# Kernel tuning notes

Measured on AMD Instinct MI355X. Metric: run time of the kernel, lower is better.

The kernel has to match this reference:

```python
import jax, jax.numpy as jnp
import numpy as np

BOUNDS = (0, 256, 384, 448, 512)  # rot_idx, trans_idx, angle_idx, embedding_dim
SCALES = [1, 2, 4, 8, 16, 32, 64]  # 2**i for i in range(scales+1), scales=6


def _pairwise_dist(q, e):
    # q: [M, C] queries, e: [K, C] codebook; per-segment squared dist / seg_dim, summed
    d = jnp.zeros((q.shape[0], e.shape[0]), dtype=q.dtype)
    for s, t in zip(BOUNDS[:-1], BOUNDS[1:]):
        qs, es = q[:, s:t], e[:, s:t]
        d = d + (jnp.sum(qs * qs, axis=1, keepdims=True)
                 + jnp.sum(es * es, axis=1)
                 - 2.0 * qs @ es.T) / (t - s)
    return d


def _elem_dist(q, k):
    # q, k: [B, C, N]; elementwise per-segment squared distance / seg_dim -> [B, N]
    d = 0.0
    for s, t in zip(BOUNDS[:-1], BOUNDS[1:]):
        diff = q[:, s:t] - k[:, s:t]
        d = d + jnp.sum(diff * diff, axis=1) / (t - s)
    return d


def _downsample_area(f, pn):
    # f: [B, C, N], pn divides N -> block-mean pooling (torch 'area')
    B, C, N = f.shape
    return f.reshape(B, C, pn, N // pn).mean(axis=-1)


def _upsample_linear(h, N):
    # h: [B, C, pn] -> [B, C, N], torch mode='linear', align_corners=False
    pn = h.shape[-1]
    src = (jnp.arange(N, dtype=jnp.float32) + 0.5) * (pn / N) - 0.5
    src = jnp.clip(src, 0.0, pn - 1)
    i0 = jnp.floor(src).astype(jnp.int32)
    i1 = jnp.minimum(i0 + 1, pn - 1)
    w = (src - i0).astype(h.dtype)
    return h[..., i0] * (1.0 - w) + h[..., i1] * w


def setup_inputs() -> dict:
    key = jax.random.key(0)
    k1, k2, k3 = jax.random.split(key, 3)
    C = 512
    f_BNC = jax.random.normal(k1, (1024, 64, C), dtype=jnp.float32)
    base = jax.random.normal(k2, (2048, C), dtype=jnp.float32)
    proj_W = jax.random.normal(k3, (C, C), dtype=jnp.float32) / np.sqrt(C)
    return {"f_BNC": f_BNC, "base": base, "proj_W": proj_W}


def reference(f_BNC, base, proj_W):
    embedding = base @ proj_W.T              # update_embedding(): proj(base)
    emb_ng = jax.lax.stop_gradient(embedding)
    f_BCN = jnp.transpose(f_BNC, (0, 2, 1))  # [B, C, N]
    B, C, N = f_BCN.shape
    f_no_grad = jax.lax.stop_gradient(f_BCN)
    f_rest = f_no_grad
    f_hat = jnp.zeros_like(f_rest)
    commit = jnp.zeros((B, N), dtype=f_BCN.dtype)
    qlat = jnp.zeros((B, N), dtype=f_BCN.dtype)
    for pn in SCALES:
        rest_NC = jnp.transpose(_downsample_area(f_rest, pn), (0, 2, 1)).reshape(-1, C)
        d = _pairwise_dist(jax.lax.stop_gradient(rest_NC), emb_ng)  # [B*pn, K]
        idx = jnp.argmin(d, axis=1)
        h_NC = embedding[idx]                                        # gather (grad -> codebook)
        h_BCn = jnp.transpose(h_NC.reshape(B, pn, C), (0, 2, 1))
        h_BCN = _upsample_linear(h_BCn, N)
        f_hat = f_hat + h_BCN
        f_rest = f_rest - h_BCN
        commit = commit + 0.25 * _elem_dist(jax.lax.stop_gradient(f_hat), f_BCN)
        qlat = qlat + _elem_dist(f_hat, f_no_grad)
    SN = float(len(SCALES))
    commit = commit / SN
    qlat = qlat / SN
    f_hat_st = jax.lax.stop_gradient(f_hat) - f_no_grad + f_BCN  # straight-through
    return (jnp.transpose(f_hat_st, (0, 2, 1)), commit, qlat)
```

## Files before the change

### kernel.cpp

```cpp
#include <hip/hip_runtime.h>

typedef __attribute__((ext_vector_type(8))) _Float16 f16x8;
typedef __attribute__((ext_vector_type(4))) float f32x4;

#define B_    1024
#define C_    512
#define NCODE 2048
#define NTOT  (B_ * 64 * C_)
#define BN_   (B_ * 64)
#define DELTA 3e-3f

__device__ __forceinline__ float wseg(int k) {
    return k < 256 ? (1.0f / 256.0f) : (k < 384 ? (1.0f / 128.0f) : (1.0f / 64.0f));
}

__global__ __launch_bounds__(256) void k_gemm_e(const float* __restrict__ A,
                                                const float* __restrict__ Bm,
                                                float* __restrict__ E) {
    __shared__ float As[16][68];
    __shared__ float Bs[16][68];
    int tid = threadIdx.x;
    int m0 = blockIdx.x * 64, n0 = blockIdx.y * 64;
    float acc[4][4] = {};
    int tx = tid & 15, ty = tid >> 4;
    int kk = tid & 15, rr = tid >> 4;
    for (int k0 = 0; k0 < 512; k0 += 16) {
        #pragma unroll
        for (int i = 0; i < 4; ++i) {
            As[kk][rr + i * 16] = A[(m0 + rr + i * 16) * 512 + k0 + kk];
            Bs[kk][rr + i * 16] = Bm[(n0 + rr + i * 16) * 512 + k0 + kk];
        }
        __syncthreads();
        #pragma unroll
        for (int k = 0; k < 16; ++k) {
            float4 a = *(const float4*)&As[k][ty * 4];
            float4 b = *(const float4*)&Bs[k][tx * 4];
            #pragma unroll
            for (int i = 0; i < 4; ++i) {
                float av = ((const float*)&a)[i];
                acc[i][0] = fmaf(av, b.x, acc[i][0]);
                acc[i][1] = fmaf(av, b.y, acc[i][1]);
                acc[i][2] = fmaf(av, b.z, acc[i][2]);
                acc[i][3] = fmaf(av, b.w, acc[i][3]);
            }
        }
        __syncthreads();
    }
    #pragma unroll
    for (int i = 0; i < 4; ++i)
        #pragma unroll
        for (int j = 0; j < 4; ++j)
            E[(m0 + ty * 4 + i) * 512 + n0 + tx * 4 + j] = acc[i][j];
}

__global__ void k_wek16(const float* __restrict__ E, _Float16* __restrict__ wk) {
    int tid = blockIdx.x * 256 + threadIdx.x;
    int k = tid & 511;
    wk[tid] = (_Float16)(E[tid] * wseg(k));
}

__global__ void k_enorm(const float* __restrict__ E, float* __restrict__ enorm) {
    int c = blockIdx.x * 256 + threadIdx.x;
    float s = 0.0f;
    for (int k = 0; k < 512; ++k) {
        float v = E[c * 512 + k];
        s = fmaf(wseg(k) * v, v, s);
    }
    enorm[c] = s;
}

__global__ __launch_bounds__(256) void k_down0(const float* __restrict__ f,
                                               _Float16* __restrict__ q16,
                                               float* __restrict__ qf) {
    int b = blockIdx.x, t = threadIdx.x;
    const float* src = f + (size_t)b * 64 * 512;
    float s0 = 0.f, s1 = 0.f;
    for (int n = 0; n < 64; ++n) {
        s0 += src[n * 512 + t];
        s1 += src[n * 512 + t + 256];
    }
    s0 *= (1.0f / 64.0f); s1 *= (1.0f / 64.0f);
    q16[(size_t)b * 512 + t] = (_Float16)s0;
    q16[(size_t)b * 512 + t + 256] = (_Float16)s1;
    qf[(size_t)b * 512 + t] = s0;
    qf[(size_t)b * 512 + t + 256] = s1;
}

__global__ __launch_bounds__(256, 4) void k_score_f16(
        const _Float16* __restrict__ q16, const _Float16* __restrict__ wek,
        const float* __restrict__ enorm, float4* __restrict__ partial) {
    __shared__ __align__(16) char smem[37376];
    float*  ensh = (float*)(smem + 32768);
    float4* bb   = (float4*)(smem + 33280);

    int tid = threadIdx.x;
    int bx = blockIdx.x;
    int m0 = blockIdx.y * 128, n0 = bx * 128;
    if (tid < 128) ensh[tid] = enorm[n0 + tid];

    int lane = tid & 63, wave = tid >> 6;
    int wrow = (wave & 1) * 64, wcol = (wave >> 1) * 64;
    int lx = lane & 15, cg = lane >> 4;

    int r0 = tid >> 2, c0 = tid & 3;
    int cs0 = (c0 ^ (r0 & 3)) * 8;
    const _Float16* gqa0 = q16 + (size_t)(m0 + r0) * 512 + cs0;
    const _Float16* gqa1 = q16 + (size_t)(m0 + 64 + r0) * 512 + cs0;
    const _Float16* gwb0 = wek + (size_t)(n0 + r0) * 512 + cs0;
    const _Float16* gwb1 = wek + (size_t)(n0 + 64 + r0) * 512 + cs0;

    #define GLL(gp, loff) __builtin_amdgcn_global_load_lds( \
        (const __attribute__((address_space(1))) unsigned int*)(gp), \
        (__attribute__((address_space(3))) unsigned int*)(smem + (loff)), 16, 0, 0)

    auto stage = [&](int p, int k0) {
        GLL(gqa0 + k0, p * 8192 + tid * 16);
        GLL(gqa1 + k0, p * 8192 + 4096 + tid * 16);
        GLL(gwb0 + k0, 16384 + p * 8192 + tid * 16);
        GLL(gwb1 + k0, 16384 + p * 8192 + 4096 + tid * 16);
    };

    f32x4 acc[4][4];
    #pragma unroll
    for (int i = 0; i < 4; ++i)
        #pragma unroll
        for (int j = 0; j < 4; ++j)
            acc[i][j] = (f32x4){0.f, 0.f, 0.f, 0.f};

    int abase = (wrow + lx) * 64 + ((cg ^ (lx & 3)) * 16);
    int bbase = (wcol + lx) * 64 + ((cg ^ (lx & 3)) * 16);

    stage(0, 0);
    __syncthreads();

    #pragma unroll
    for (int ks = 0; ks < 16; ++ks) {
        int p = ks & 1;
        if (ks < 15) stage(p ^ 1, (ks + 1) * 32);
        f16x8 af[4], bf[4];
        #pragma unroll
        for (int i = 0; i < 4; ++i) {
            af[i] = *(const f16x8*)(smem + p * 8192 + abase + i * 1024);
            bf[i] = *(const f16x8*)(smem + 16384 + p * 8192 + bbase + i * 1024);
        }
        #pragma unroll
        for (int i = 0; i < 4; ++i)
            #pragma unroll
            for (int j = 0; j < 4; ++j)
                acc[i][j] = __builtin_amdgcn_mfma_f32_16x16x32_f16(af[i], bf[j], acc[i][j], 0, 0, 0);
        __syncthreads();
    }

    #pragma unroll
    for (int fi = 0; fi < 4; ++fi) {
        #pragma unroll
        for (int r = 0; r < 4; ++r) {
            float v1 = INFINITY, v2 = INFINITY; int i1 = NCODE, i2 = NCODE;
            #pragma unroll
            for (int fj = 0; fj < 4; ++fj) {
                int nl = wcol + fj * 16 + lx;
                float s = ensh[nl] - 2.0f * acc[fi][fj][r];
                int code = n0 + nl;
                if (s < v1) { v2 = v1; i2 = i1; v1 = s; i1 = code; }
                else if (s < v2) { v2 = s; i2 = code; }
            }
            #pragma unroll
            for (int d = 1; d < 16; d <<= 1) {
                float ov1 = __shfl_xor(v1, d), ov2 = __shfl_xor(v2, d);
                int oi1 = __shfl_xor(i1, d), oi2 = __shfl_xor(i2, d);
                if (ov1 < v1) {
                    if (v1 < ov2) { v2 = v1; i2 = i1; } else { v2 = ov2; i2 = oi2; }
                    v1 = ov1; i1 = oi1;
                } else if (ov1 < v2) { v2 = ov1; i2 = oi1; }
            }
            if (lx == 0) {
                int row = wrow + fi * 16 + cg * 4 + r;
                bb[row * 2 + (wave >> 1)] = make_float4(v1, __int_as_float(i1),
                                                        v2, __int_as_float(i2));
            }
        }
    }
    __syncthreads();
    if (tid < 128) {
        float4 A4 = bb[tid * 2], C4 = bb[tid * 2 + 1];
        float v1, v2; int i1, i2;
        if (A4.x <= C4.x) {
            v1 = A4.x; i1 = __float_as_int(A4.y);
            if (A4.z <= C4.x) { v2 = A4.z; i2 = __float_as_int(A4.w); }
            else { v2 = C4.x; i2 = __float_as_int(C4.y); }
        } else {
            v1 = C4.x; i1 = __float_as_int(C4.y);
            if (C4.z <= A4.x) { v2 = C4.z; i2 = __float_as_int(C4.w); }
            else { v2 = A4.x; i2 = __float_as_int(A4.y); }
        }
        partial[(size_t)(m0 + tid) * 16 + bx] =
            make_float4(v1, __int_as_float(i1), v2, __int_as_float(i2));
    }
}

__global__ __launch_bounds__(256) void k_rescue(
        const float4* __restrict__ partial, const float* __restrict__ qf,
        const float* __restrict__ E, const float* __restrict__ enorm,
        int* __restrict__ idxb) {
    int wid = (blockIdx.x * 256 + threadIdx.x) >> 6;
    int lane = threadIdx.x & 63;
    float4 p;
    if (lane < 16) p = partial[(size_t)wid * 16 + lane];
    else p = make_float4(INFINITY, __int_as_float(NCODE), INFINITY, __int_as_float(NCODE));
    float bv = p.x;
    #pragma unroll
    for (int d = 1; d < 64; d <<= 1) bv = fminf(bv, __shfl_xor(bv, d));
    float thresh = bv + DELTA;
    unsigned long long m1 = __ballot(lane < 16 && p.x <= thresh);
    unsigned long long m2 = __ballot(lane < 16 && p.z <= thresh);
    const float* q = qf + (size_t)wid * 512 + lane * 8;
    float4 q0 = *(const float4*)q;
    float4 q1 = *(const float4*)(q + 4);
    float w = wseg(lane * 8);
    float qw0 = q0.x * w, qw1 = q0.y * w, qw2 = q0.z * w, qw3 = q0.w * w;
    float qw4 = q1.x * w, qw5 = q1.y * w, qw6 = q1.z * w, qw7 = q1.w * w;
    float bs = INFINITY; int bi = NCODE;
    while (m1 | m2) {
        int ci;
        if (m1) {
            int src = __ffsll((long long)m1) - 1; m1 &= m1 - 1;
            ci = __shfl(__float_as_int(p.y), src);
        } else {
            int src = __ffsll((long long)m2) - 1; m2 &= m2 - 1;
            ci = __shfl(__float_as_int(p.w), src);
        }
        const float* e = E + (size_t)ci * 512 + lane * 8;
        float4 e0 = *(const float4*)e;
        float4 e1 = *(const float4*)(e + 4);
        float a = 0.f;
        a = fmaf(qw0, e0.x, a); a = fmaf(qw1, e0.y, a);
        a = fmaf(qw2, e0.z, a); a = fmaf(qw3, e0.w, a);
        a = fmaf(qw4, e1.x, a); a = fmaf(qw5, e1.y, a);
        a = fmaf(qw6, e1.z, a); a = fmaf(qw7, e1.w, a);
        #pragma unroll
        for (int d = 1; d < 64; d <<= 1) a += __shfl_xor(a, d);
        float s = enorm[ci] - 2.0f * a;
        if (s < bs || (s == bs && ci < bi)) { bs = s; bi = ci; }
    }
    if (lane == 0) idxb[wid] = bi;
}

__global__ __launch_bounds__(256) void k_update(
        const float* __restrict__ E, const int* __restrict__ idx,
        const float* __restrict__ f, float* __restrict__ rest,
        float* __restrict__ dacc, _Float16* __restrict__ q16n,
        float* __restrict__ qf32n, int pn, int sn, int mode) {
    int t = threadIdx.x;
    int pn_next = 1 << sn;
    int r = 64 >> sn;
    int b = blockIdx.x >> sn;
    int chunk = blockIdx.x & (pn_next - 1);
    float w0 = wseg(t), w1 = wseg(t + 256);
    float macc0 = 0.f, macc1 = 0.f;
    float pscale = (float)pn * (1.0f / 64.0f);
    __shared__ float redw[4];
    for (int ri = 0; ri < r; ++ri) {
        int n = chunk * r + ri;
        int row = (b << 6) + n;
        float srcp = fminf(fmaxf((n + 0.5f) * pscale - 0.5f, 0.0f), (float)(pn - 1));
        int i0 = (int)floorf(srcp);
        int i1 = min(i0 + 1, pn - 1);
        float wl = srcp - (float)i0;
        int cc0 = idx[b * pn + i0];
        int cc1 = idx[b * pn + i1];
        const float* e0 = E + (size_t)cc0 * 512;
        const float* e1 = E + (size_t)cc1 * 512;
        const float* rs = (mode & 1) ? f + (size_t)row * 512 : rest + (size_t)row * 512;
        float s = 0.f;
        {
            float h = (1.0f - wl) * e0[t] + wl * e1[t];
            float v = rs[t] - h;
            rest[(size_t)row * 512 + t] = (mode & 2) ? (f[(size_t)row * 512 + t] - v) : v;
            s = fmaf(w0 * v, v, s);
            macc0 += v;
        }
        {
            int c = t + 256;
            float h = (1.0f - wl) * e0[c] + wl * e1[c];
            float v = rs[c] - h;
            rest[(size_t)row * 512 + c] = (mode & 2) ? (f[(size_t)row * 512 + c] - v) : v;
            s = fmaf(w1 * v, v, s);
            macc1 += v;
        }
        #pragma unroll
        for (int d = 1; d < 64; d <<= 1) s += __shfl_xor(s, d);
        if ((t & 63) == 0) redw[t >> 6] = s;
        __syncthreads();
        if (t == 0) {
            float tot = redw[0] + redw[1] + redw[2] + redw[3];
            dacc[row] = (mode & 1) ? tot : dacc[row] + tot;
        }
        __syncthreads();
    }
    if (!(mode & 2)) {
        float inv = 1.0f / (float)r;
        size_t qrow = ((size_t)b << sn) + chunk;
        float m0v = macc0 * inv, m1v = macc1 * inv;
        q16n[qrow * 512 + t] = (_Float16)m0v;
        q16n[qrow * 512 + t + 256] = (_Float16)m1v;
        if (mode & 4) {
            qf32n[qrow * 512 + t] = m0v;
            qf32n[qrow * 512 + t + 256] = m1v;
        }
    }
}

__global__ void k_out12(const float* __restrict__ dacc, float* __restrict__ out) {
    int i = blockIdx.x * 256 + threadIdx.x;
    float d = dacc[i];
    out[i] = d * (0.25f / 7.0f);
    out[BN_ + i] = d * (1.0f / 7.0f);
}

extern "C" void kernel_launch(void* const* d_in, const int* in_sizes, int n_in,
                              void* d_out, int out_size, void* d_ws, size_t ws_size,
                              hipStream_t stream) {
    const float* f    = (const float*)d_in[0];
    const float* base = (const float*)d_in[1];
    const float* W    = (const float*)d_in[2];
    float* out = (float*)d_out;
    float* rest = out;

    char* ws = (char*)d_ws;
    float*     E      = (float*)ws;     ws += (size_t)NCODE * 512 * 4;
    _Float16*  wek16  = (_Float16*)ws;  ws += (size_t)NCODE * 512 * 2;
    _Float16*  q16a   = (_Float16*)ws;  ws += (size_t)32768 * 512 * 2;
    char*      big64  = ws;             ws += (size_t)65536 * 512 * 2;
    float4*    partial= (float4*)ws;    ws += (size_t)65536 * 16 * 16;
    float*     dacc   = (float*)ws;     ws += (size_t)BN_ * 4;
    int*       idxb   = (int*)ws;       ws += (size_t)BN_ * 4;
    float*     enorm  = (float*)ws;     ws += (size_t)NCODE * 4;

    k_gemm_e<<<dim3(NCODE / 64, 512 / 64), 256, 0, stream>>>(base, W, E);
    k_wek16<<<(NCODE * 512) / 256, 256, 0, stream>>>(E, wek16);
    k_enorm<<<NCODE / 256, 256, 0, stream>>>(E, enorm);
    k_down0<<<B_, 256, 0, stream>>>(f, q16a, (float*)big64);

    const int scales[7] = {1, 2, 4, 8, 16, 32, 64};
    for (int si = 0; si < 7; ++si) {
        int pn = scales[si];
        int M = 1024 * pn;
        const _Float16* q16s = (pn == 64) ? (const _Float16*)big64 : q16a;
        const float*    qfs  = (pn == 64) ? rest : (const float*)big64;

        k_score_f16<<<dim3(16, M / 128), 256, 0, stream>>>(q16s, wek16, enorm, partial);
        k_rescue<<<M / 4, 256, 0, stream>>>(partial, qfs, E, enorm, idxb);

        int pn_next = (si == 6) ? 64 : pn * 2;
        int sn = 0; while ((1 << sn) != pn_next) ++sn;
        int mode = (si == 0 ? 1 : 0) | (si == 6 ? 2 : 0) | ((si <= 4) ? 4 : 0);
        _Float16* q16n = (pn_next == 64) ? (_Float16*)big64 : q16a;
        k_update<<<1024 * pn_next, 256, 0, stream>>>(E, idxb, f, rest, dacc,
                                                     q16n, (float*)big64, pn, sn, mode);
    }

    k_out12<<<BN_ / 256, 256, 0, stream>>>(dacc, out + NTOT);
}
```

Baseline: 1.210 ms.

## Loop over all codebook tiles per block with running top-2 in registers

The score kernel now has each block own 128 query rows and walk all 16 codebook tiles itself, reading operands straight from global memory with no LDS staging. It keeps a per-lane running top-2 in registers and writes 32 partial candidates per row with no shuffle or LDS reduction. The rescue kernel now scans 32 candidates, and at the last scale the partial buffer reuses the q16a region to save workspace. This cuts partial-buffer traffic and per-tile epilogue work, but loses shared-memory reuse and double buffering, and the first scale launches only 8 blocks.

```diff
diff --git a/kernel.cpp b/kernel.cpp
--- a/kernel.cpp
+++ b/kernel.cpp
@@ -86,116 +86,85 @@
     qf[(size_t)b * 512 + t + 256] = s1;
 }
 
-__global__ __launch_bounds__(256, 4) void k_score_f16(
+__global__ __launch_bounds__(256) void k_score_f16(
         const _Float16* __restrict__ q16, const _Float16* __restrict__ wek,
         const float* __restrict__ enorm, float4* __restrict__ partial) {
-    __shared__ __align__(16) char smem[37376];
-    float*  ensh = (float*)(smem + 32768);
-    float4* bb   = (float4*)(smem + 33280);
-
     int tid = threadIdx.x;
-    int bx = blockIdx.x;
-    int m0 = blockIdx.y * 128, n0 = bx * 128;
-    if (tid < 128) ensh[tid] = enorm[n0 + tid];
-
+    int m0 = blockIdx.x * 128;
     int lane = tid & 63, wave = tid >> 6;
     int wrow = (wave & 1) * 64, wcol = (wave >> 1) * 64;
     int lx = lane & 15, cg = lane >> 4;
 
-    int r0 = tid >> 2, c0 = tid & 3;
-    int cs0 = (c0 ^ (r0 & 3)) * 8;
-    const _Float16* gqa0 = q16 + (size_t)(m0 + r0) * 512 + cs0;
-    const _Float16* gqa1 = q16 + (size_t)(m0 + 64 + r0) * 512 + cs0;
-    const _Float16* gwb0 = wek + (size_t)(n0 + r0) * 512 + cs0;
-    const _Float16* gwb1 = wek + (size_t)(n0 + 64 + r0) * 512 + cs0;
-
-    #define GLL(gp, loff) __builtin_amdgcn_global_load_lds( \
-        (const __attribute__((address_space(1))) unsigned int*)(gp), \
-        (__attribute__((address_space(3))) unsigned int*)(smem + (loff)), 16, 0, 0)
-
-    auto stage = [&](int p, int k0) {
-        GLL(gqa0 + k0, p * 8192 + tid * 16);
-        GLL(gqa1 + k0, p * 8192 + 4096 + tid * 16);
-        GLL(gwb0 + k0, 16384 + p * 8192 + tid * 16);
-        GLL(gwb1 + k0, 16384 + p * 8192 + 4096 + tid * 16);
-    };
-
-    f32x4 acc[4][4];
+    const _Float16* Ap = q16 + (size_t)(m0 + wrow + lx) * 512 + cg * 8;
+    const _Float16* Bp = wek + (size_t)(wcol + lx) * 512 + cg * 8;
+
+    float v1[4][4], v2[4][4]; int i1[4][4], i2[4][4];
     #pragma unroll
-    for (int i = 0; i < 4; ++i)
-        #pragma unroll
-        for (int j = 0; j < 4; ++j)
-            acc[i][j] = (f32x4){0.f, 0.f, 0.f, 0.f};
-
-    int abase = (wrow + lx) * 64 + ((cg ^ (lx & 3)) * 16);
-    int bbase = (wcol + lx) * 64 + ((cg ^ (lx & 3)) * 16);
-
-    stage(0, 0);
-    __syncthreads();
-
+    for (int a = 0; a < 4; ++a)
+        #pragma unroll
+        for (int b = 0; b < 4; ++b) {
+            v1[a][b] = INFINITY; v2[a][b] = INFINITY;
+            i1[a][b] = NCODE; i2[a][b] = NCODE;
+        }
+
+    #pragma unroll 1
+    for (int ct = 0; ct < 16; ++ct) {
+        float en[4];
+        #pragma unroll
+        for (int fj = 0; fj < 4; ++fj)
+            en[fj] = enorm[ct * 128 + wcol + fj * 16 + lx];
+
+        f32x4 acc[4][4];
+        #pragma unroll
+        for (int i = 0; i < 4; ++i)
+            #pragma unroll
+            for (int j = 0; j < 4; ++j)
+                acc[i][j] = (f32x4){0.f, 0.f, 0.f, 0.f};
+
+        const _Float16* Bc = Bp + (size_t)ct * 128 * 512;
+        #pragma unroll
+        for (int ks = 0; ks < 16; ++ks) {
+            f16x8 af[4], bf[4];
+            #pragma unroll
+            for (int i = 0; i < 4; ++i) {
+                af[i] = *(const f16x8*)(Ap + i * 16 * 512 + ks * 32);
+                bf[i] = *(const f16x8*)(Bc + i * 16 * 512 + ks * 32);
+            }
+            #pragma unroll
+            for (int i = 0; i < 4; ++i)
+                #pragma unroll
+                for (int j = 0; j < 4; ++j)
+                    acc[i][j] = __builtin_amdgcn_mfma_f32_16x16x32_f16(af[i], bf[j], acc[i][j], 0, 0, 0);
+        }
+
+        #pragma unroll
+        for (int fi = 0; fi < 4; ++fi)
+            #pragma unroll
+            for (int fj = 0; fj < 4; ++fj) {
+                int code = ct * 128 + wcol + fj * 16 + lx;
+                #pragma unroll
+                for (int r = 0; r < 4; ++r) {
+                    float s = fmaf(-2.0f, acc[fi][fj][r], en[fj]);
+                    if (s < v1[fi][r]) {
+                        v2[fi][r] = v1[fi][r]; i2[fi][r] = i1[fi][r];
+                        v1[fi][r] = s; i1[fi][r] = code;
+                    } else if (s < v2[fi][r]) {
+                        v2[fi][r] = s; i2[fi][r] = code;
+                    }
+                }
+            }
+    }
+
+    int slot = (wave >> 1) * 16 + lx;
     #pragma unroll
-    for (int ks = 0; ks < 16; ++ks) {
-        int p = ks & 1;
-        if (ks < 15) stage(p ^ 1, (ks + 1) * 32);
-        f16x8 af[4], bf[4];
-        #pragma unroll
-        for (int i = 0; i < 4; ++i) {
-            af[i] = *(const f16x8*)(smem + p * 8192 + abase + i * 1024);
-            bf[i] = *(const f16x8*)(smem + 16384 + p * 8192 + bbase + i * 1024);
-        }
-        #pragma unroll
-        for (int i = 0; i < 4; ++i)
-            #pragma unroll
-            for (int j = 0; j < 4; ++j)
-                acc[i][j] = __builtin_amdgcn_mfma_f32_16x16x32_f16(af[i], bf[j], acc[i][j], 0, 0, 0);
-        __syncthreads();
-    }
-
-    #pragma unroll
-    for (int fi = 0; fi < 4; ++fi) {
+    for (int fi = 0; fi < 4; ++fi)
         #pragma unroll
         for (int r = 0; r < 4; ++r) {
-            float v1 = INFINITY, v2 = INFINITY; int i1 = NCODE, i2 = NCODE;
-            #pragma unroll
-            for (int fj = 0; fj < 4; ++fj) {
-                int nl = wcol + fj * 16 + lx;
-                float s = ensh[nl] - 2.0f * acc[fi][fj][r];
-                int code = n0 + nl;
-                if (s < v1) { v2 = v1; i2 = i1; v1 = s; i1 = code; }
-                else if (s < v2) { v2 = s; i2 = code; }
-            }
-            #pragma unroll
-            for (int d = 1; d < 16; d <<= 1) {
-                float ov1 = __shfl_xor(v1, d), ov2 = __shfl_xor(v2, d);
-                int oi1 = __shfl_xor(i1, d), oi2 = __shfl_xor(i2, d);
-                if (ov1 < v1) {
-                    if (v1 < ov2) { v2 = v1; i2 = i1; } else { v2 = ov2; i2 = oi2; }
-                    v1 = ov1; i1 = oi1;
-                } else if (ov1 < v2) { v2 = ov1; i2 = oi1; }
-            }
-            if (lx == 0) {
-                int row = wrow + fi * 16 + cg * 4 + r;
-                bb[row * 2 + (wave >> 1)] = make_float4(v1, __int_as_float(i1),
-                                                        v2, __int_as_float(i2));
-            }
-        }
-    }
-    __syncthreads();
-    if (tid < 128) {
-        float4 A4 = bb[tid * 2], C4 = bb[tid * 2 + 1];
-        float v1, v2; int i1, i2;
-        if (A4.x <= C4.x) {
-            v1 = A4.x; i1 = __float_as_int(A4.y);
-            if (A4.z <= C4.x) { v2 = A4.z; i2 = __float_as_int(A4.w); }
-            else { v2 = C4.x; i2 = __float_as_int(C4.y); }
-        } else {
-            v1 = C4.x; i1 = __float_as_int(C4.y);
-            if (C4.z <= A4.x) { v2 = C4.z; i2 = __float_as_int(C4.w); }
-            else { v2 = A4.x; i2 = __float_as_int(A4.y); }
-        }
-        partial[(size_t)(m0 + tid) * 16 + bx] =
-            make_float4(v1, __int_as_float(i1), v2, __int_as_float(i2));
-    }
+            int row = wrow + fi * 16 + cg * 4 + r;
+            partial[(size_t)(m0 + row) * 32 + slot] =
+                make_float4(v1[fi][r], __int_as_float(i1[fi][r]),
+                            v2[fi][r], __int_as_float(i2[fi][r]));
+        }
 }
 
 __global__ __launch_bounds__(256) void k_rescue(
@@ -205,14 +174,14 @@
     int wid = (blockIdx.x * 256 + threadIdx.x) >> 6;
     int lane = threadIdx.x & 63;
     float4 p;
-    if (lane < 16) p = partial[(size_t)wid * 16 + lane];
+    if (lane < 32) p = partial[(size_t)wid * 32 + lane];
     else p = make_float4(INFINITY, __int_as_float(NCODE), INFINITY, __int_as_float(NCODE));
     float bv = p.x;
     #pragma unroll
     for (int d = 1; d < 64; d <<= 1) bv = fminf(bv, __shfl_xor(bv, d));
     float thresh = bv + DELTA;
-    unsigned long long m1 = __ballot(lane < 16 && p.x <= thresh);
-    unsigned long long m2 = __ballot(lane < 16 && p.z <= thresh);
+    unsigned long long m1 = __ballot(lane < 32 && p.x <= thresh);
+    unsigned long long m2 = __ballot(lane < 32 && p.z <= thresh);
     const float* q = qf + (size_t)wid * 512 + lane * 8;
     float4 q0 = *(const float4*)q;
     float4 q1 = *(const float4*)(q + 4);
@@ -331,7 +300,7 @@
     _Float16*  wek16  = (_Float16*)ws;  ws += (size_t)NCODE * 512 * 2;
     _Float16*  q16a   = (_Float16*)ws;  ws += (size_t)32768 * 512 * 2;
     char*      big64  = ws;             ws += (size_t)65536 * 512 * 2;
-    float4*    partial= (float4*)ws;    ws += (size_t)65536 * 16 * 16;
+    float4*    partS  = (float4*)ws;    ws += (size_t)32768 * 32 * 16;
     float*     dacc   = (float*)ws;     ws += (size_t)BN_ * 4;
     int*       idxb   = (int*)ws;       ws += (size_t)BN_ * 4;
     float*     enorm  = (float*)ws;     ws += (size_t)NCODE * 4;
@@ -347,9 +316,10 @@
         int M = 1024 * pn;
         const _Float16* q16s = (pn == 64) ? (const _Float16*)big64 : q16a;
         const float*    qfs  = (pn == 64) ? rest : (const float*)big64;
-
-        k_score_f16<<<dim3(16, M / 128), 256, 0, stream>>>(q16s, wek16, enorm, partial);
-        k_rescue<<<M / 4, 256, 0, stream>>>(partial, qfs, E, enorm, idxb);
+        float4*         part = (pn == 64) ? (float4*)q16a : partS;
+
+        k_score_f16<<<M / 128, 256, 0, stream>>>(q16s, wek16, enorm, part);
+        k_rescue<<<M / 4, 256, 0, stream>>>(part, qfs, E, enorm, idxb);
 
         int pn_next = (si == 6) ? 64 : pn * 2;
         int sn = 0; while ((1 << sn) != pn_next) ++sn;
```

After: 2.872 ms. 137% more time.

## Triple-buffer score GEMM LDS pipeline with vmcnt waits and MFMA priority

Applied to the files above, without the earlier changes.

Converts the f16 score GEMM's LDS staging from double to triple buffering, prefetching two K-steps ahead and replacing __syncthreads with explicit vmcnt waits plus a single barrier per step. It also changes the LDS XOR swizzle to use row bits 2-3, and raises wave priority around the MFMA block. The goal is to hide global-to-LDS latency and cut the barrier cost per step. In exchange it uses more shared memory and drops the occupancy hint of 4 blocks per CU, so fewer blocks may stay resident.

```diff
diff --git a/kernel.cpp b/kernel.cpp
--- a/kernel.cpp
+++ b/kernel.cpp
@@ -86,12 +86,12 @@
     qf[(size_t)b * 512 + t + 256] = s1;
 }
 
-__global__ __launch_bounds__(256, 4) void k_score_f16(
+__global__ __launch_bounds__(256) void k_score_f16(
         const _Float16* __restrict__ q16, const _Float16* __restrict__ wek,
         const float* __restrict__ enorm, float4* __restrict__ partial) {
-    __shared__ __align__(16) char smem[37376];
-    float*  ensh = (float*)(smem + 32768);
-    float4* bb   = (float4*)(smem + 33280);
+    __shared__ __align__(16) char smem[49152 + 512 + 4096];
+    float*  ensh = (float*)(smem + 49152);
+    float4* bb   = (float4*)(smem + 49152 + 512);
 
     int tid = threadIdx.x;
     int bx = blockIdx.x;
@@ -103,7 +103,7 @@
     int lx = lane & 15, cg = lane >> 4;
 
     int r0 = tid >> 2, c0 = tid & 3;
-    int cs0 = (c0 ^ (r0 & 3)) * 8;
+    int cs0 = (c0 ^ ((r0 >> 2) & 3)) * 8;
     const _Float16* gqa0 = q16 + (size_t)(m0 + r0) * 512 + cs0;
     const _Float16* gqa1 = q16 + (size_t)(m0 + 64 + r0) * 512 + cs0;
     const _Float16* gwb0 = wek + (size_t)(n0 + r0) * 512 + cs0;
@@ -113,11 +113,11 @@
         (const __attribute__((address_space(1))) unsigned int*)(gp), \
         (__attribute__((address_space(3))) unsigned int*)(smem + (loff)), 16, 0, 0)
 
-    auto stage = [&](int p, int k0) {
-        GLL(gqa0 + k0, p * 8192 + tid * 16);
-        GLL(gqa1 + k0, p * 8192 + 4096 + tid * 16);
-        GLL(gwb0 + k0, 16384 + p * 8192 + tid * 16);
-        GLL(gwb1 + k0, 16384 + p * 8192 + 4096 + tid * 16);
+    auto stage = [&](int buf, int k0) {
+        GLL(gqa0 + k0, buf * 16384 + tid * 16);
+        GLL(gqa1 + k0, buf * 16384 + 4096 + tid * 16);
+        GLL(gwb0 + k0, buf * 16384 + 8192 + tid * 16);
+        GLL(gwb1 + k0, buf * 16384 + 12288 + tid * 16);
     };
 
     f32x4 acc[4][4];
@@ -127,28 +127,35 @@
         for (int j = 0; j < 4; ++j)
             acc[i][j] = (f32x4){0.f, 0.f, 0.f, 0.f};
 
-    int abase = (wrow + lx) * 64 + ((cg ^ (lx & 3)) * 16);
-    int bbase = (wcol + lx) * 64 + ((cg ^ (lx & 3)) * 16);
+    int swz = (cg ^ ((lx >> 2) & 3)) * 16;
+    int abase = (wrow + lx) * 64 + swz;
+    int bbase = 8192 + (wcol + lx) * 64 + swz;
 
     stage(0, 0);
-    __syncthreads();
+    stage(1, 32);
 
     #pragma unroll
     for (int ks = 0; ks < 16; ++ks) {
-        int p = ks & 1;
-        if (ks < 15) stage(p ^ 1, (ks + 1) * 32);
+        int buf = ks % 3;
+        if (ks < 15) asm volatile("s_waitcnt vmcnt(4)" ::: "memory");
+        else         asm volatile("s_waitcnt vmcnt(0)" ::: "memory");
+        __builtin_amdgcn_s_barrier();
+        asm volatile("" ::: "memory");
+        if (ks < 14) stage((ks + 2) % 3, (ks + 2) * 32);
         f16x8 af[4], bf[4];
         #pragma unroll
         for (int i = 0; i < 4; ++i) {
-            af[i] = *(const f16x8*)(smem + p * 8192 + abase + i * 1024);
-            bf[i] = *(const f16x8*)(smem + 16384 + p * 8192 + bbase + i * 1024);
-        }
+            af[i] = *(const f16x8*)(smem + buf * 16384 + abase + i * 1024);
+            bf[i] = *(const f16x8*)(smem + buf * 16384 + bbase + i * 1024);
+        }
+        __builtin_amdgcn_s_setprio(1);
         #pragma unroll
         for (int i = 0; i < 4; ++i)
             #pragma unroll
             for (int j = 0; j < 4; ++j)
                 acc[i][j] = __builtin_amdgcn_mfma_f32_16x16x32_f16(af[i], bf[j], acc[i][j], 0, 0, 0);
-        __syncthreads();
+        __builtin_amdgcn_s_setprio(0);
+        asm volatile("" ::: "memory");
     }
 
     #pragma unroll
```

Result: slower. 1.240 ms (+2.4%).

## Remap score GEMM blocks to a grouped 1D grid and re-swizzle LDS tiles

Applied to the files above, without the earlier changes.

The score kernel now launches a 1D grid and decodes it so that eight consecutive blocks share one codebook column tile while covering eight query row tiles. This is meant to improve L2 reuse of the codebook and query tiles. The LDS layout is also reorganised: each buffer interleaves A and B, the rows are arranged differently, and the XOR swizzle widens from 4 to 8 chunks to reduce bank conflicts. The launch-bounds occupancy hint of 4 is dropped, which may change register allocation and occupancy.

```diff
diff --git a/kernel.cpp b/kernel.cpp
--- a/kernel.cpp
+++ b/kernel.cpp
@@ -86,7 +86,7 @@
     qf[(size_t)b * 512 + t + 256] = s1;
 }
 
-__global__ __launch_bounds__(256, 4) void k_score_f16(
+__global__ __launch_bounds__(256) void k_score_f16(
         const _Float16* __restrict__ q16, const _Float16* __restrict__ wek,
         const float* __restrict__ enorm, float4* __restrict__ partial) {
     __shared__ __align__(16) char smem[37376];
@@ -94,30 +94,35 @@
     float4* bb   = (float4*)(smem + 33280);
 
     int tid = threadIdx.x;
-    int bx = blockIdx.x;
-    int m0 = blockIdx.y * 128, n0 = bx * 128;
+    int x = blockIdx.x;
+    int bx = (x >> 3) & 15;
+    int g  = (x & 7) + ((x >> 7) << 3);
+    int m0 = g * 128, n0 = bx * 128;
     if (tid < 128) ensh[tid] = enorm[n0 + tid];
 
     int lane = tid & 63, wave = tid >> 6;
     int wrow = (wave & 1) * 64, wcol = (wave >> 1) * 64;
     int lx = lane & 15, cg = lane >> 4;
 
-    int r0 = tid >> 2, c0 = tid & 3;
-    int cs0 = (c0 ^ (r0 & 3)) * 8;
-    const _Float16* gqa0 = q16 + (size_t)(m0 + r0) * 512 + cs0;
-    const _Float16* gqa1 = q16 + (size_t)(m0 + 64 + r0) * 512 + cs0;
-    const _Float16* gwb0 = wek + (size_t)(n0 + r0) * 512 + cs0;
-    const _Float16* gwb1 = wek + (size_t)(n0 + 64 + r0) * 512 + cs0;
+    int u = (tid & 7) ^ ((tid >> 3) & 7);
+    int chunk = u & 3;
+    int rhi = (u >> 2) << 6;
+    int r0 = (tid >> 3) + rhi;
+    int r1 = 32 + (tid >> 3) + rhi;
+    const _Float16* gqa0 = q16 + (size_t)(m0 + r0) * 512 + chunk * 8;
+    const _Float16* gqa1 = q16 + (size_t)(m0 + r1) * 512 + chunk * 8;
+    const _Float16* gwb0 = wek + (size_t)(n0 + r0) * 512 + chunk * 8;
+    const _Float16* gwb1 = wek + (size_t)(n0 + r1) * 512 + chunk * 8;
 
     #define GLL(gp, loff) __builtin_amdgcn_global_load_lds( \
         (const __attribute__((address_space(1))) unsigned int*)(gp), \
         (__attribute__((address_space(3))) unsigned int*)(smem + (loff)), 16, 0, 0)
 
-    auto stage = [&](int p, int k0) {
-        GLL(gqa0 + k0, p * 8192 + tid * 16);
-        GLL(gqa1 + k0, p * 8192 + 4096 + tid * 16);
-        GLL(gwb0 + k0, 16384 + p * 8192 + tid * 16);
-        GLL(gwb1 + k0, 16384 + p * 8192 + 4096 + tid * 16);
+    auto stage = [&](int buf, int k0) {
+        GLL(gqa0 + k0, buf * 16384 + tid * 16);
+        GLL(gqa1 + k0, buf * 16384 + 4096 + tid * 16);
+        GLL(gwb0 + k0, buf * 16384 + 8192 + tid * 16);
+        GLL(gwb1 + k0, buf * 16384 + 12288 + tid * 16);
     };
 
     f32x4 acc[4][4];
@@ -127,8 +132,10 @@
         for (int j = 0; j < 4; ++j)
             acc[i][j] = (f32x4){0.f, 0.f, 0.f, 0.f};
 
-    int abase = (wrow + lx) * 64 + ((cg ^ (lx & 3)) * 16);
-    int bbase = (wcol + lx) * 64 + ((cg ^ (lx & 3)) * 16);
+    int swzA = (((wrow >> 6) * 4 + cg) ^ (lx & 7)) * 16;
+    int swzB = (((wcol >> 6) * 4 + cg) ^ (lx & 7)) * 16;
+    int abase = lx * 128 + swzA;
+    int bbase = 8192 + lx * 128 + swzB;
 
     stage(0, 0);
     __syncthreads();
@@ -140,8 +147,8 @@
         f16x8 af[4], bf[4];
         #pragma unroll
         for (int i = 0; i < 4; ++i) {
-            af[i] = *(const f16x8*)(smem + p * 8192 + abase + i * 1024);
-            bf[i] = *(const f16x8*)(smem + 16384 + p * 8192 + bbase + i * 1024);
+            af[i] = *(const f16x8*)(smem + p * 16384 + abase + i * 2048);
+            bf[i] = *(const f16x8*)(smem + p * 16384 + bbase + i * 2048);
         }
         #pragma unroll
         for (int i = 0; i < 4; ++i)
@@ -348,7 +355,7 @@
         const _Float16* q16s = (pn == 64) ? (const _Float16*)big64 : q16a;
         const float*    qfs  = (pn == 64) ? rest : (const float*)big64;
 
-        k_score_f16<<<dim3(16, M / 128), 256, 0, stream>>>(q16s, wek16, enorm, partial);
+        k_score_f16<<<16 * (M / 128), 256, 0, stream>>>(q16s, wek16, enorm, partial);
         k_rescue<<<M / 4, 256, 0, stream>>>(partial, qfs, E, enorm, idxb);
 
         int pn_next = (si == 6) ? 64 : pn * 2;
```

Result: no change. 1.226 ms (+1.3%).
